# Kernel optimization log

Hardware: AMD Instinct MI355X
Metric: run time of the kernel (lower is better)

Reference implementation:

```python
import jax, jax.numpy as jnp
import numpy as np

N = 8192        # nodes
NFEAT = 256     # input feature dim
NHID = 64       # per-head hidden dim
NHEADS = 4
NCLASS = 121    # PPI label count
ALPHA = 0.2     # LeakyReLU negative slope
NEG_INF = jnp.float32(-9e15)  # pyGAT's mask fill value


def setup_inputs() -> dict:
    key = jax.random.key(0)
    k = jax.random.split(key, 6)
    x = jax.random.normal(k[0], (N, NFEAT), dtype=jnp.float32)
    adj = (jax.random.uniform(k[1], (N, N)) < 0.01).astype(jnp.float32)
    idx = jnp.arange(N)
    adj = adj.at[idx, idx].set(1.0)
    # per-head first-layer params: W [H, nfeat, nhid], a [H, 2*nhid]
    Ws = jax.random.normal(k[2], (NHEADS, NFEAT, NHID), dtype=jnp.float32) * 0.1
    a_heads = jax.random.normal(k[3], (NHEADS, 2 * NHID), dtype=jnp.float32) * 0.1
    # output attention layer params
    W_out = jax.random.normal(k[4], (NHEADS * NHID, NCLASS), dtype=jnp.float32) * 0.1
    a_out = jax.random.normal(k[5], (2 * NCLASS,), dtype=jnp.float32) * 0.1
    return {"x": x, "adj": adj, "Ws": Ws, "a_heads": a_heads,
            "W_out": W_out, "a_out": a_out}


def _gat_head(x, adj, W, a, concat):
    # Dense GraphAttentionLayer (pyGAT), eval mode (dropout off).
    Wh = x @ W                                   # [N, d]
    d = W.shape[1]
    f_src = Wh @ a[:d]                           # [N]  score contribution of node i
    f_dst = Wh @ a[d:]                           # [N]  score contribution of node j
    e = jax.nn.leaky_relu(f_src[:, None] + f_dst[None, :], ALPHA)  # [N, N]
    e = jnp.where(adj > 0, e, NEG_INF)
    att = jax.nn.softmax(e, axis=-1)             # [N, N]
    h = att @ Wh                                 # [N, d]
    return jax.nn.elu(h) if concat else h


def reference(x, adj, Ws, a_heads, W_out, a_out):
    # first multi-head layer (concat=True, elu), vmapped over heads
    heads = jax.vmap(lambda W, a: _gat_head(x, adj, W, a, True))(Ws, a_heads)  # [H, N, nhid]
    h_cat = jnp.transpose(heads, (1, 0, 2)).reshape(x.shape[0], NHEADS * NHID)  # torch.cat(dim=1)
    # output attention layer (concat=False -> raw aggregation)
    return _gat_head(h_cat, adj, W_out, a_out, False)  # [N, nclass]
```

## Files before the change

kernel.cpp:

```cpp
#include <hip/hip_runtime.h>
#include <math.h>

#define N_NODES 8192
#define NFEAT 256
#define NHID 64
#define NHEADS 4
#define NCLASS 121
#define NCPAD 128
#define CAP 256
#define LRALPHA 0.2f

typedef float f32x4 __attribute__((ext_vector_type(4)));
typedef _Float16 f16;
typedef _Float16 f16x4 __attribute__((ext_vector_type(4)));

__device__ __forceinline__ float lrelu(float x) { return x > 0.f ? x : LRALPHA * x; }
__device__ __forceinline__ f32x4 splat4(float v) { f32x4 r = {v, v, v, v}; return r; }

__global__ __launch_bounds__(256) void build_csr(const float* __restrict__ adj,
                                                 int* __restrict__ nbr,
                                                 int* __restrict__ deg) {
    int row = blockIdx.x;
    __shared__ int cnt;
    if (threadIdx.x == 0) cnt = 0;
    __syncthreads();
    const f32x4* arow = (const f32x4*)(adj + (size_t)row * N_NODES);
    for (int j4 = threadIdx.x; j4 < N_NODES / 4; j4 += 256) {
        f32x4 v = __builtin_nontemporal_load(&arow[j4]);
        if (v.x > 0.f) { int s = atomicAdd(&cnt, 1); if (s < CAP) nbr[row * CAP + s] = j4 * 4 + 0; }
        if (v.y > 0.f) { int s = atomicAdd(&cnt, 1); if (s < CAP) nbr[row * CAP + s] = j4 * 4 + 1; }
        if (v.z > 0.f) { int s = atomicAdd(&cnt, 1); if (s < CAP) nbr[row * CAP + s] = j4 * 4 + 2; }
        if (v.w > 0.f) { int s = atomicAdd(&cnt, 1); if (s < CAP) nbr[row * CAP + s] = j4 * 4 + 3; }
    }
    __syncthreads();
    if (threadIdx.x == 0) deg[row] = cnt < CAP ? cnt : CAP;
}

__global__ __launch_bounds__(256) void pad_params(const float* __restrict__ Wout,
                                                  const float* __restrict__ aout,
                                                  float* __restrict__ Wpad,
                                                  float* __restrict__ apad) {
    int idx = blockIdx.x * 256 + threadIdx.x;
    if (idx < 256 * NCPAD) {
        int k = idx >> 7, c = idx & 127;
        Wpad[idx] = (c < NCLASS) ? Wout[k * NCLASS + c] : 0.f;
    }
    if (idx < 256) {
        int c = idx & 127;
        float v = 0.f;
        if (c < NCLASS) v = (idx < 128) ? aout[c] : aout[NCLASS + c];
        apad[idx] = v;
    }
}

__global__ __launch_bounds__(256) void gemm1(const float* __restrict__ x,
                                             const float* __restrict__ Ws,
                                             f16* __restrict__ Wh1h) {
    int h = blockIdx.y;
    int r0 = blockIdx.x * 64;
    __shared__ float xs[64][260];
    for (int t = threadIdx.x; t < 64 * 64; t += 256) {
        int r = t >> 6, c4 = t & 63;
        *(float4*)&xs[r][c4 * 4] = *(const float4*)(x + (size_t)(r0 + r) * NFEAT + c4 * 4);
    }
    __syncthreads();
    int d = threadIdx.x & 63;
    int rb = (threadIdx.x >> 6) * 16;
    const float* W = Ws + (size_t)h * NFEAT * NHID + d;
    float acc[16] = {};
    for (int k4 = 0; k4 < NFEAT; k4 += 4) {
        float b0 = W[(k4 + 0) * NHID];
        float b1 = W[(k4 + 1) * NHID];
        float b2 = W[(k4 + 2) * NHID];
        float b3 = W[(k4 + 3) * NHID];
#pragma unroll
        for (int r = 0; r < 16; r++) {
            float4 a = *(const float4*)&xs[rb + r][k4];
            acc[r] += a.x * b0 + a.y * b1 + a.z * b2 + a.w * b3;
        }
    }
#pragma unroll
    for (int r = 0; r < 16; r++)
        Wh1h[(size_t)(r0 + rb + r) * (NHEADS * NHID) + h * NHID + d] = (f16)acc[r];
}

__global__ __launch_bounds__(256) void attn_coef1(const f16* __restrict__ Wh1h,
                                                  const float* __restrict__ a_heads,
                                                  float* __restrict__ fs1t,
                                                  float* __restrict__ fd1t) {
    int i = blockIdx.x;
    int h = threadIdx.x >> 6, lane = threadIdx.x & 63;
    float wh = (float)Wh1h[(size_t)i * (NHEADS * NHID) + h * NHID + lane];
    float s = wh * a_heads[h * 2 * NHID + lane];
    float dd = wh * a_heads[h * 2 * NHID + NHID + lane];
#pragma unroll
    for (int o = 32; o > 0; o >>= 1) { s += __shfl_down(s, o); dd += __shfl_down(dd, o); }
    if (lane == 0) { fs1t[i * 4 + h] = s; fd1t[i * 4 + h] = dd; }
}

__global__ __launch_bounds__(256) void attn_agg1(const int* __restrict__ nbr,
                                                 const int* __restrict__ deg,
                                                 const f16* __restrict__ Wh1h,
                                                 const float* __restrict__ fs1t,
                                                 const float* __restrict__ fd1t,
                                                 float* __restrict__ hcat) {
    int w = threadIdx.x >> 6, lane = threadIdx.x & 63;
    int i = blockIdx.x * 4 + w;
    __shared__ int nbrs[4][CAP];
    __shared__ float pbuf[4][CAP][4];
    int dg = deg[i];
    for (int t = lane; t < dg; t += 64)
        nbrs[w][t] = nbr[i * CAP + t];
    f32x4 fsi = *(const f32x4*)(fs1t + (size_t)i * 4);
    f32x4 e[4];
    f32x4 m4 = splat4(-3.4e38f);
#pragma unroll
    for (int k = 0; k < 4; k++) {
        int t = lane + (k << 6);
        if (t < dg) {
            int j = nbrs[w][t];
            f32x4 fdj = *(const f32x4*)(fd1t + (size_t)j * 4);
            f32x4 ev;
            ev.x = lrelu(fsi.x + fdj.x);
            ev.y = lrelu(fsi.y + fdj.y);
            ev.z = lrelu(fsi.z + fdj.z);
            ev.w = lrelu(fsi.w + fdj.w);
            e[k] = ev;
            m4.x = fmaxf(m4.x, ev.x); m4.y = fmaxf(m4.y, ev.y);
            m4.z = fmaxf(m4.z, ev.z); m4.w = fmaxf(m4.w, ev.w);
        }
    }
#pragma unroll
    for (int o = 32; o > 0; o >>= 1) {
        m4.x = fmaxf(m4.x, __shfl_xor(m4.x, o));
        m4.y = fmaxf(m4.y, __shfl_xor(m4.y, o));
        m4.z = fmaxf(m4.z, __shfl_xor(m4.z, o));
        m4.w = fmaxf(m4.w, __shfl_xor(m4.w, o));
    }
    f32x4 s4 = splat4(0.f);
#pragma unroll
    for (int k = 0; k < 4; k++) {
        int t = lane + (k << 6);
        if (t < dg) {
            f32x4 p;
            p.x = __expf(e[k].x - m4.x);
            p.y = __expf(e[k].y - m4.y);
            p.z = __expf(e[k].z - m4.z);
            p.w = __expf(e[k].w - m4.w);
            *(f32x4*)&pbuf[w][t][0] = p;
            s4 += p;
        }
    }
#pragma unroll
    for (int o = 32; o > 0; o >>= 1) {
        s4.x += __shfl_xor(s4.x, o);
        s4.y += __shfl_xor(s4.y, o);
        s4.z += __shfl_xor(s4.z, o);
        s4.w += __shfl_xor(s4.w, o);
    }
    __syncthreads();
    int hl = lane >> 4;
    const f16* wrow = Wh1h + 4 * lane;
    f32x4 acc = splat4(0.f);
#pragma unroll 8
    for (int t = 0; t < dg; t++) {
        int j = nbrs[w][t];
        float p = pbuf[w][t][hl];
        f16x4 wv = *(const f16x4*)(wrow + (size_t)j * (NHEADS * NHID));
        acc += __builtin_convertvector(wv, f32x4) * splat4(p);
    }
    float sh = hl == 0 ? s4.x : hl == 1 ? s4.y : hl == 2 ? s4.z : s4.w;
    acc.x /= sh; acc.y /= sh; acc.z /= sh; acc.w /= sh;
    acc.x = acc.x > 0.f ? acc.x : expm1f(acc.x);
    acc.y = acc.y > 0.f ? acc.y : expm1f(acc.y);
    acc.z = acc.z > 0.f ? acc.z : expm1f(acc.z);
    acc.w = acc.w > 0.f ? acc.w : expm1f(acc.w);
    *(f32x4*)(hcat + (size_t)i * (NHEADS * NHID) + 4 * lane) = acc;
}

__global__ __launch_bounds__(256) void gemm2(const float* __restrict__ hcat,
                                             const float* __restrict__ Wpad,
                                             f16* __restrict__ Wh2h) {
    int r0 = blockIdx.x * 64;
    __shared__ float xs[64][260];
    for (int t = threadIdx.x; t < 64 * 64; t += 256) {
        int r = t >> 6, c4 = t & 63;
        *(float4*)&xs[r][c4 * 4] = *(const float4*)(hcat + (size_t)(r0 + r) * 256 + c4 * 4);
    }
    __syncthreads();
    int c0 = (threadIdx.x & 63) * 2;
    int rb = (threadIdx.x >> 6) * 16;
    float acc0[16] = {}, acc1[16] = {};
    for (int k4 = 0; k4 < 256; k4 += 4) {
        float2 b0 = *(const float2*)&Wpad[(k4 + 0) * NCPAD + c0];
        float2 b1 = *(const float2*)&Wpad[(k4 + 1) * NCPAD + c0];
        float2 b2 = *(const float2*)&Wpad[(k4 + 2) * NCPAD + c0];
        float2 b3 = *(const float2*)&Wpad[(k4 + 3) * NCPAD + c0];
#pragma unroll
        for (int r = 0; r < 16; r++) {
            float4 a = *(const float4*)&xs[rb + r][k4];
            acc0[r] += a.x * b0.x + a.y * b1.x + a.z * b2.x + a.w * b3.x;
            acc1[r] += a.x * b0.y + a.y * b1.y + a.z * b2.y + a.w * b3.y;
        }
    }
#pragma unroll
    for (int r = 0; r < 16; r++) {
        f16 v0 = (f16)acc0[r], v1 = (f16)acc1[r];
        f16* p = &Wh2h[(size_t)(r0 + rb + r) * NCPAD + c0];
        p[0] = v0; p[1] = v1;
    }
}

__global__ __launch_bounds__(256) void attn_coef2(const f16* __restrict__ Wh2h,
                                                  const float* __restrict__ apad,
                                                  float* __restrict__ fs2,
                                                  float* __restrict__ fd2) {
    int i = blockIdx.x * 4 + (threadIdx.x >> 6);
    int lane = threadIdx.x & 63;
    float w0 = (float)Wh2h[(size_t)i * NCPAD + lane];
    float w1 = (float)Wh2h[(size_t)i * NCPAD + 64 + lane];
    float s = w0 * apad[lane] + w1 * apad[64 + lane];
    float dd = w0 * apad[128 + lane] + w1 * apad[192 + lane];
#pragma unroll
    for (int o = 32; o > 0; o >>= 1) { s += __shfl_down(s, o); dd += __shfl_down(dd, o); }
    if (lane == 0) { fs2[i] = s; fd2[i] = dd; }
}

__global__ __launch_bounds__(256) void attn_agg2(const int* __restrict__ nbr,
                                                 const int* __restrict__ deg,
                                                 const f16* __restrict__ Wh2h,
                                                 const float* __restrict__ fs2,
                                                 const float* __restrict__ fd2,
                                                 float* __restrict__ out) {
    int w = threadIdx.x >> 6, lane = threadIdx.x & 63;
    int i = blockIdx.x * 4 + w;
    __shared__ int nbrs[4][CAP];
    __shared__ float pbuf[4][CAP];
    int dg = deg[i];
    for (int t = lane; t < dg; t += 64)
        nbrs[w][t] = nbr[i * CAP + t];
    float fsi = fs2[i];
    float e[4];
    float m = -3.4e38f;
#pragma unroll
    for (int k = 0; k < 4; k++) {
        int t = lane + (k << 6);
        if (t < dg) {
            float ev = lrelu(fsi + fd2[nbrs[w][t]]);
            e[k] = ev;
            m = fmaxf(m, ev);
        }
    }
#pragma unroll
    for (int o = 32; o > 0; o >>= 1) m = fmaxf(m, __shfl_xor(m, o));
    float s = 0.f;
#pragma unroll
    for (int k = 0; k < 4; k++) {
        int t = lane + (k << 6);
        if (t < dg) {
            float p = __expf(e[k] - m);
            pbuf[w][t] = p;
            s += p;
        }
    }
#pragma unroll
    for (int o = 32; o > 0; o >>= 1) s += __shfl_xor(s, o);
    __syncthreads();
    int eg = lane >> 5, c = lane & 31;
    const f16* wrow = Wh2h + 4 * c;
    f32x4 acc = splat4(0.f);
#pragma unroll 4
    for (int tt = 0; tt < dg; tt += 2) {
        int t = tt + eg;
        int tc = t < dg ? t : 0;
        float p = t < dg ? pbuf[w][tc] : 0.f;
        int j = nbrs[w][tc];
        f16x4 wv = *(const f16x4*)(wrow + (size_t)j * NCPAD);
        acc += __builtin_convertvector(wv, f32x4) * splat4(p);
    }
    acc.x += __shfl_xor(acc.x, 32);
    acc.y += __shfl_xor(acc.y, 32);
    acc.z += __shfl_xor(acc.z, 32);
    acc.w += __shfl_xor(acc.w, 32);
    if (eg == 0) {
        int c4 = c * 4;
#pragma unroll
        for (int q = 0; q < 4; q++)
            if (c4 + q < NCLASS) out[(size_t)i * NCLASS + c4 + q] = acc[q] / s;
    }
}


extern "C" void kernel_launch(void* const* d_in, const int* in_sizes, int n_in,
                              void* d_out, int out_size, void* d_ws, size_t ws_size,
                              hipStream_t stream) {
    const float* x       = (const float*)d_in[0];
    const float* adj     = (const float*)d_in[1];
    const float* Ws      = (const float*)d_in[2];
    const float* a_heads = (const float*)d_in[3];
    const float* Wout    = (const float*)d_in[4];
    const float* aout    = (const float*)d_in[5];
    float* out = (float*)d_out;

    char* ws = (char*)d_ws;
    size_t off = 0;
    auto alloc = [&](size_t bytes) { void* p = ws + off; off = (off + bytes + 255) & ~(size_t)255; return p; };
    int*   nbr  = (int*)  alloc((size_t)N_NODES * CAP * 4);
    int*   deg  = (int*)  alloc((size_t)N_NODES * 4);
    f16*   Wh1h = (f16*)  alloc((size_t)N_NODES * NHEADS * NHID * 2);
    float* fs1t = (float*)alloc((size_t)N_NODES * 4 * 4);
    float* fd1t = (float*)alloc((size_t)N_NODES * 4 * 4);
    float* hcat = (float*)alloc((size_t)N_NODES * NHEADS * NHID * 4);
    f16*   Wh2h = (f16*)  alloc((size_t)N_NODES * NCPAD * 2);
    float* fs2  = (float*)alloc((size_t)N_NODES * 4);
    float* fd2  = (float*)alloc((size_t)N_NODES * 4);
    float* Wpad = (float*)alloc((size_t)256 * NCPAD * 4);
    float* apad = (float*)alloc((size_t)256 * 4);

    build_csr<<<N_NODES, 256, 0, stream>>>(adj, nbr, deg);
    pad_params<<<128, 256, 0, stream>>>(Wout, aout, Wpad, apad);
    gemm1<<<dim3(N_NODES / 64, NHEADS), 256, 0, stream>>>(x, Ws, Wh1h);
    attn_coef1<<<N_NODES, 256, 0, stream>>>(Wh1h, a_heads, fs1t, fd1t);
    attn_agg1<<<N_NODES / 4, 256, 0, stream>>>(nbr, deg, Wh1h, fs1t, fd1t, hcat);
    gemm2<<<N_NODES / 64, 256, 0, stream>>>(hcat, Wpad, Wh2h);
    attn_coef2<<<N_NODES / 4, 256, 0, stream>>>(Wh2h, apad, fs2, fd2);
    attn_agg2<<<N_NODES / 4, 256, 0, stream>>>(nbr, deg, Wh2h, fs2, fd2, out);
}
```

Measured before the change: 497.5 us.

## Fuse CSR build, param padding, GEMM1 and coef1 into one kernel; fuse GEMM2 with coef2

CSR construction, parameter padding, the first per-head GEMM and its attention-coefficient computation now run in a single 1024-block kernel. The GEMM blocks reduce f_src/f_dst straight from fp32 accumulators with wave shuffles, and every block then grid-strides over adjacency rows. The second GEMM likewise computes fs2/fd2 in its epilogue instead of in a separate kernel. This removes several launches and the re-reads of Wh1h/Wh2h, but the adjacency scan now shares a 66KB-LDS kernel, which may lower occupancy for the bandwidth-bound scan.

```diff
diff --git a/kernel.cpp b/kernel.cpp
--- a/kernel.cpp
+++ b/kernel.cpp
@@ -17,85 +17,84 @@
 __device__ __forceinline__ float lrelu(float x) { return x > 0.f ? x : LRALPHA * x; }
 __device__ __forceinline__ f32x4 splat4(float v) { f32x4 r = {v, v, v, v}; return r; }
 
-__global__ __launch_bounds__(256) void build_csr(const float* __restrict__ adj,
-                                                 int* __restrict__ nbr,
-                                                 int* __restrict__ deg) {
-    int row = blockIdx.x;
-    __shared__ int cnt;
-    if (threadIdx.x == 0) cnt = 0;
-    __syncthreads();
-    const f32x4* arow = (const f32x4*)(adj + (size_t)row * N_NODES);
-    for (int j4 = threadIdx.x; j4 < N_NODES / 4; j4 += 256) {
-        f32x4 v = __builtin_nontemporal_load(&arow[j4]);
-        if (v.x > 0.f) { int s = atomicAdd(&cnt, 1); if (s < CAP) nbr[row * CAP + s] = j4 * 4 + 0; }
-        if (v.y > 0.f) { int s = atomicAdd(&cnt, 1); if (s < CAP) nbr[row * CAP + s] = j4 * 4 + 1; }
-        if (v.z > 0.f) { int s = atomicAdd(&cnt, 1); if (s < CAP) nbr[row * CAP + s] = j4 * 4 + 2; }
-        if (v.w > 0.f) { int s = atomicAdd(&cnt, 1); if (s < CAP) nbr[row * CAP + s] = j4 * 4 + 3; }
-    }
-    __syncthreads();
-    if (threadIdx.x == 0) deg[row] = cnt < CAP ? cnt : CAP;
-}
-
-__global__ __launch_bounds__(256) void pad_params(const float* __restrict__ Wout,
-                                                  const float* __restrict__ aout,
-                                                  float* __restrict__ Wpad,
-                                                  float* __restrict__ apad) {
-    int idx = blockIdx.x * 256 + threadIdx.x;
-    if (idx < 256 * NCPAD) {
-        int k = idx >> 7, c = idx & 127;
-        Wpad[idx] = (c < NCLASS) ? Wout[k * NCLASS + c] : 0.f;
-    }
-    if (idx < 256) {
-        int c = idx & 127;
-        float v = 0.f;
-        if (c < NCLASS) v = (idx < 128) ? aout[c] : aout[NCLASS + c];
-        apad[idx] = v;
-    }
-}
-
-__global__ __launch_bounds__(256) void gemm1(const float* __restrict__ x,
-                                             const float* __restrict__ Ws,
-                                             f16* __restrict__ Wh1h) {
-    int h = blockIdx.y;
-    int r0 = blockIdx.x * 64;
-    __shared__ float xs[64][260];
-    for (int t = threadIdx.x; t < 64 * 64; t += 256) {
-        int r = t >> 6, c4 = t & 63;
-        *(float4*)&xs[r][c4 * 4] = *(const float4*)(x + (size_t)(r0 + r) * NFEAT + c4 * 4);
-    }
-    __syncthreads();
-    int d = threadIdx.x & 63;
-    int rb = (threadIdx.x >> 6) * 16;
-    const float* W = Ws + (size_t)h * NFEAT * NHID + d;
-    float acc[16] = {};
-    for (int k4 = 0; k4 < NFEAT; k4 += 4) {
-        float b0 = W[(k4 + 0) * NHID];
-        float b1 = W[(k4 + 1) * NHID];
-        float b2 = W[(k4 + 2) * NHID];
-        float b3 = W[(k4 + 3) * NHID];
+__global__ __launch_bounds__(256) void phaseA(
+    const float* __restrict__ x, const float* __restrict__ adj,
+    const float* __restrict__ Ws, const float* __restrict__ a_heads,
+    const float* __restrict__ Wout, const float* __restrict__ aout,
+    int* __restrict__ nbr, int* __restrict__ deg,
+    f16* __restrict__ Wh1h, float* __restrict__ fs1t, float* __restrict__ fd1t,
+    float* __restrict__ Wpad, float* __restrict__ apad)
+{
+    __shared__ union { float xs[64][260]; int cnt; } sm;
+    const int tid = threadIdx.x;
+
+    if (blockIdx.x < 512) {
+        int h = blockIdx.x & 3;
+        int r0 = (blockIdx.x >> 2) * 64;
+        for (int t = tid; t < 64 * 64; t += 256) {
+            int r = t >> 6, c4 = t & 63;
+            *(float4*)&sm.xs[r][c4 * 4] = *(const float4*)(x + (size_t)(r0 + r) * NFEAT + c4 * 4);
+        }
+        __syncthreads();
+        int d = tid & 63;
+        int rb = (tid >> 6) * 16;
+        const float* W = Ws + (size_t)h * NFEAT * NHID + d;
+        float acc[16] = {};
+        for (int k4 = 0; k4 < NFEAT; k4 += 4) {
+            float b0 = W[(k4 + 0) * NHID];
+            float b1 = W[(k4 + 1) * NHID];
+            float b2 = W[(k4 + 2) * NHID];
+            float b3 = W[(k4 + 3) * NHID];
+#pragma unroll
+            for (int r = 0; r < 16; r++) {
+                float4 a = *(const float4*)&sm.xs[rb + r][k4];
+                acc[r] += a.x * b0 + a.y * b1 + a.z * b2 + a.w * b3;
+            }
+        }
+        float ah_s = a_heads[h * 2 * NHID + d];
+        float ah_d = a_heads[h * 2 * NHID + NHID + d];
 #pragma unroll
         for (int r = 0; r < 16; r++) {
-            float4 a = *(const float4*)&xs[rb + r][k4];
-            acc[r] += a.x * b0 + a.y * b1 + a.z * b2 + a.w * b3;
-        }
-    }
-#pragma unroll
-    for (int r = 0; r < 16; r++)
-        Wh1h[(size_t)(r0 + rb + r) * (NHEADS * NHID) + h * NHID + d] = (f16)acc[r];
-}
-
-__global__ __launch_bounds__(256) void attn_coef1(const f16* __restrict__ Wh1h,
-                                                  const float* __restrict__ a_heads,
-                                                  float* __restrict__ fs1t,
-                                                  float* __restrict__ fd1t) {
-    int i = blockIdx.x;
-    int h = threadIdx.x >> 6, lane = threadIdx.x & 63;
-    float wh = (float)Wh1h[(size_t)i * (NHEADS * NHID) + h * NHID + lane];
-    float s = wh * a_heads[h * 2 * NHID + lane];
-    float dd = wh * a_heads[h * 2 * NHID + NHID + lane];
-#pragma unroll
-    for (int o = 32; o > 0; o >>= 1) { s += __shfl_down(s, o); dd += __shfl_down(dd, o); }
-    if (lane == 0) { fs1t[i * 4 + h] = s; fd1t[i * 4 + h] = dd; }
+            int row = r0 + rb + r;
+            Wh1h[(size_t)row * (NHEADS * NHID) + h * NHID + d] = (f16)acc[r];
+            float s = acc[r] * ah_s;
+            float dd = acc[r] * ah_d;
+#pragma unroll
+            for (int o = 32; o > 0; o >>= 1) { s += __shfl_xor(s, o); dd += __shfl_xor(dd, o); }
+            if (d == 0) { fs1t[(size_t)row * 4 + h] = s; fd1t[(size_t)row * 4 + h] = dd; }
+        }
+        __syncthreads();
+    }
+
+    for (int row = blockIdx.x; row < N_NODES; row += gridDim.x) {
+        if (tid == 0) sm.cnt = 0;
+        __syncthreads();
+        const f32x4* arow = (const f32x4*)(adj + (size_t)row * N_NODES);
+        for (int j4 = tid; j4 < N_NODES / 4; j4 += 256) {
+            f32x4 v = __builtin_nontemporal_load(&arow[j4]);
+            if (v.x > 0.f) { int s = atomicAdd(&sm.cnt, 1); if (s < CAP) nbr[row * CAP + s] = j4 * 4 + 0; }
+            if (v.y > 0.f) { int s = atomicAdd(&sm.cnt, 1); if (s < CAP) nbr[row * CAP + s] = j4 * 4 + 1; }
+            if (v.z > 0.f) { int s = atomicAdd(&sm.cnt, 1); if (s < CAP) nbr[row * CAP + s] = j4 * 4 + 2; }
+            if (v.w > 0.f) { int s = atomicAdd(&sm.cnt, 1); if (s < CAP) nbr[row * CAP + s] = j4 * 4 + 3; }
+        }
+        __syncthreads();
+        if (tid == 0) deg[row] = sm.cnt < CAP ? sm.cnt : CAP;
+        __syncthreads();
+    }
+
+    {
+        int idx = blockIdx.x * 256 + tid;
+        if (idx < 256 * NCPAD) {
+            int k = idx >> 7, c = idx & 127;
+            Wpad[idx] = (c < NCLASS) ? Wout[k * NCLASS + c] : 0.f;
+        }
+        if (blockIdx.x == 0) {
+            int c = tid & 127;
+            float v = 0.f;
+            if (c < NCLASS) v = (tid < 128) ? aout[c] : aout[NCLASS + c];
+            apad[tid] = v;
+        }
+    }
 }
 
 __global__ __launch_bounds__(256) void attn_agg1(const int* __restrict__ nbr,
@@ -178,9 +177,12 @@
     *(f32x4*)(hcat + (size_t)i * (NHEADS * NHID) + 4 * lane) = acc;
 }
 
-__global__ __launch_bounds__(256) void gemm2(const float* __restrict__ hcat,
-                                             const float* __restrict__ Wpad,
-                                             f16* __restrict__ Wh2h) {
+__global__ __launch_bounds__(256) void phaseC(const float* __restrict__ hcat,
+                                              const float* __restrict__ Wpad,
+                                              const float* __restrict__ apad,
+                                              f16* __restrict__ Wh2h,
+                                              float* __restrict__ fs2,
+                                              float* __restrict__ fd2) {
     int r0 = blockIdx.x * 64;
     __shared__ float xs[64][260];
     for (int t = threadIdx.x; t < 64 * 64; t += 256) {
@@ -203,27 +205,19 @@
             acc1[r] += a.x * b0.y + a.y * b1.y + a.z * b2.y + a.w * b3.y;
         }
     }
+    float as0 = apad[c0], as1 = apad[c0 + 1];
+    float ad0 = apad[128 + c0], ad1 = apad[128 + c0 + 1];
 #pragma unroll
     for (int r = 0; r < 16; r++) {
-        f16 v0 = (f16)acc0[r], v1 = (f16)acc1[r];
-        f16* p = &Wh2h[(size_t)(r0 + rb + r) * NCPAD + c0];
-        p[0] = v0; p[1] = v1;
-    }
-}
-
-__global__ __launch_bounds__(256) void attn_coef2(const f16* __restrict__ Wh2h,
-                                                  const float* __restrict__ apad,
-                                                  float* __restrict__ fs2,
-                                                  float* __restrict__ fd2) {
-    int i = blockIdx.x * 4 + (threadIdx.x >> 6);
-    int lane = threadIdx.x & 63;
-    float w0 = (float)Wh2h[(size_t)i * NCPAD + lane];
-    float w1 = (float)Wh2h[(size_t)i * NCPAD + 64 + lane];
-    float s = w0 * apad[lane] + w1 * apad[64 + lane];
-    float dd = w0 * apad[128 + lane] + w1 * apad[192 + lane];
-#pragma unroll
-    for (int o = 32; o > 0; o >>= 1) { s += __shfl_down(s, o); dd += __shfl_down(dd, o); }
-    if (lane == 0) { fs2[i] = s; fd2[i] = dd; }
+        int row = r0 + rb + r;
+        f16* p = &Wh2h[(size_t)row * NCPAD + c0];
+        p[0] = (f16)acc0[r]; p[1] = (f16)acc1[r];
+        float s = acc0[r] * as0 + acc1[r] * as1;
+        float dd = acc0[r] * ad0 + acc1[r] * ad1;
+#pragma unroll
+        for (int o = 32; o > 0; o >>= 1) { s += __shfl_xor(s, o); dd += __shfl_xor(dd, o); }
+        if ((threadIdx.x & 63) == 0) { fs2[row] = s; fd2[row] = dd; }
+    }
 }
 
 __global__ __launch_bounds__(256) void attn_agg2(const int* __restrict__ nbr,
@@ -317,12 +311,9 @@
     float* Wpad = (float*)alloc((size_t)256 * NCPAD * 4);
     float* apad = (float*)alloc((size_t)256 * 4);
 
-    build_csr<<<N_NODES, 256, 0, stream>>>(adj, nbr, deg);
-    pad_params<<<128, 256, 0, stream>>>(Wout, aout, Wpad, apad);
-    gemm1<<<dim3(N_NODES / 64, NHEADS), 256, 0, stream>>>(x, Ws, Wh1h);
-    attn_coef1<<<N_NODES, 256, 0, stream>>>(Wh1h, a_heads, fs1t, fd1t);
+    phaseA<<<1024, 256, 0, stream>>>(x, adj, Ws, a_heads, Wout, aout,
+                                     nbr, deg, Wh1h, fs1t, fd1t, Wpad, apad);
     attn_agg1<<<N_NODES / 4, 256, 0, stream>>>(nbr, deg, Wh1h, fs1t, fd1t, hcat);
-    gemm2<<<N_NODES / 64, 256, 0, stream>>>(hcat, Wpad, Wh2h);
-    attn_coef2<<<N_NODES / 4, 256, 0, stream>>>(Wh2h, apad, fs2, fd2);
+    phaseC<<<N_NODES / 64, 256, 0, stream>>>(hcat, Wpad, apad, Wh2h, fs2, fd2);
     attn_agg2<<<N_NODES / 4, 256, 0, stream>>>(nbr, deg, Wh2h, fs2, fd2, out);
 }
```

Measured after the change: 560.4 us. 12.6% more time.
